# Performance work log

Measured on AMD Instinct MI355X. Metric: run time of the kernel, lower is better.

The kernel has to match this reference:

```python
import jax, jax.numpy as jnp
import numpy as np

N_NODES = 100000
N_EDGES = 600000
IN_DIM = 128
HID = 128


def setup_inputs() -> dict:
    key = jax.random.key(0)
    ks = jax.random.split(key, 9)
    x = jax.random.normal(ks[0], (N_NODES, IN_DIM), dtype=jnp.float32)
    edge_index = jax.random.randint(ks[1], (2, N_EDGES), 0, N_NODES, dtype=jnp.int64)
    s = 1.0 / np.sqrt(IN_DIM)
    # PyG SAGEConv: out = lin_l(mean_aggr(x_src)) + lin_r(x_root); lin_l carries the bias.
    W_l0 = jax.random.uniform(ks[2], (IN_DIM, HID), jnp.float32, -s, s)
    b_l0 = jnp.zeros((HID,), jnp.float32)
    W_r0 = jax.random.uniform(ks[3], (IN_DIM, HID), jnp.float32, -s, s)
    s2 = 1.0 / np.sqrt(HID)
    W_l1 = jax.random.uniform(ks[4], (HID, HID), jnp.float32, -s2, s2)
    b_l1 = jnp.zeros((HID,), jnp.float32)
    W_r1 = jax.random.uniform(ks[5], (HID, HID), jnp.float32, -s2, s2)
    return {"x": x, "edge_index": edge_index,
            "W_l0": W_l0, "b_l0": b_l0, "W_r0": W_r0,
            "W_l1": W_l1, "b_l1": b_l1, "W_r1": W_r1}


def _sage_mean_conv(h, src, dst, W_l, b_l, W_r):
    # gather source-node features per edge, scatter-mean into destinations
    msgs = h[src]                                              # [E, D]
    sums = jax.ops.segment_sum(msgs, dst, num_segments=N_NODES)  # [N, D]
    cnt = jax.ops.segment_sum(jnp.ones((src.shape[0],), h.dtype), dst,
                              num_segments=N_NODES)             # [N]
    mean = sums / jnp.maximum(cnt, 1.0)[:, None]
    return mean @ W_l + b_l + h @ W_r


def reference(x, edge_index, W_l0, b_l0, W_r0, W_l1, b_l1, W_r1):
    src, dst = edge_index[0], edge_index[1]
    h = _sage_mean_conv(x, src, dst, W_l0, b_l0, W_r0)
    h = jax.nn.relu(h)  # dropout is identity in eval mode
    h = _sage_mean_conv(h, src, dst, W_l1, b_l1, W_r1)
    h = jax.nn.relu(h)
    return h
```

## Files before the change

kernel.cpp:

```cpp
#include <hip/hip_runtime.h>

#define N_NODES 100000
#define N_EDGES 600000
#define DIM 128

typedef __attribute__((ext_vector_type(8))) short bf16x8;
typedef __attribute__((ext_vector_type(4))) float f32x4;

typedef __attribute__((address_space(1))) const unsigned int g_u32;
typedef __attribute__((address_space(3))) unsigned int l_u32;
__device__ __forceinline__ void stage16(const void* g, void* l) {
  __builtin_amdgcn_global_load_lds((g_u32*)g, (l_u32*)l, 16, 0, 0);
}

__device__ __forceinline__ unsigned short f32_to_bf16_rn(float f) {
  unsigned int u = __builtin_bit_cast(unsigned int, f);
  unsigned int r = (u + 0x7FFFu + ((u >> 16) & 1u)) >> 16;
  return (unsigned short)r;
}

__global__ __launch_bounds__(256) void prep_k(
    const float* __restrict__ Wl0, const float* __restrict__ Wr0,
    const float* __restrict__ Wl1, const float* __restrict__ Wr1,
    unsigned short* __restrict__ P0, unsigned short* __restrict__ P1,
    const float* __restrict__ x, unsigned short* __restrict__ xhi,
    int* __restrict__ deg) {
  const int gid = blockIdx.x * 256 + threadIdx.x;
  if (gid < N_NODES) deg[gid] = 0;
  if (gid < 65536) {
    const int layer = gid >> 15;
    const int idx = gid & 32767;
    const int j = idx & 7;
    const int l = (idx >> 3) & 63;
    const int nt = (idx >> 9) & 7;
    const int g = idx >> 12;
    const int k = ((g & 3) << 5) + ((l >> 4) << 3) + j;
    const int n = (nt << 4) + (l & 15);
    const float* W = layer ? ((g < 4) ? Wl1 : Wr1) : ((g < 4) ? Wl0 : Wr0);
    (layer ? P1 : P0)[idx] = f32_to_bf16_rn(W[k * 128 + n]);
  } else {
    const int i = gid - 65536;
    if (i < N_NODES * DIM / 4) {
      const float4 v = reinterpret_cast<const float4*>(x)[i];
      const float f[4] = {v.x, v.y, v.z, v.w};
      unsigned short h[4];
#pragma unroll
      for (int j = 0; j < 4; ++j) h[j] = f32_to_bf16_rn(f[j]);
      uint2 hp;
      hp.x = (unsigned)h[0] | ((unsigned)h[1] << 16);
      hp.y = (unsigned)h[2] | ((unsigned)h[3] << 16);
      reinterpret_cast<uint2*>(xhi)[i] = hp;
    }
  }
}

__global__ void hist_k(const int* __restrict__ dst, int* __restrict__ deg) {
  int e = blockIdx.x * blockDim.x + threadIdx.x;
  if (e < N_EDGES) atomicAdd(&deg[dst[e]], 1);
}

__global__ __launch_bounds__(1024) void scan1_k(const int* __restrict__ deg,
                                                int* __restrict__ incl,
                                                int* __restrict__ bsum) {
  __shared__ int wsum[16];
  const int t = threadIdx.x, lane = t & 63, w = t >> 6;
  const int gi = blockIdx.x * 1024 + t;
  int v = (gi < N_NODES) ? deg[gi] : 0;
  int s = v;
#pragma unroll
  for (int off = 1; off < 64; off <<= 1) {
    int u = __shfl_up(s, off);
    if (lane >= off) s += u;
  }
  if (lane == 63) wsum[w] = s;
  __syncthreads();
  if (t < 16) {
    int ws = wsum[t];
#pragma unroll
    for (int off = 1; off < 16; off <<= 1) {
      int u = __shfl_up(ws, off);
      if (t >= off) ws += u;
    }
    wsum[t] = ws;
  }
  __syncthreads();
  const int val = s + (w ? wsum[w - 1] : 0);
  if (gi < N_NODES) incl[gi] = val;
  if (t == 1023) bsum[blockIdx.x] = val;
}

__global__ void scan2_k(const int* __restrict__ bsum, int* __restrict__ boffs,
                        int nb) {
  __shared__ int w0;
  const int t = threadIdx.x;
  int v = (t < nb) ? bsum[t] : 0;
  int s = v;
#pragma unroll
  for (int off = 1; off < 64; off <<= 1) {
    int u = __shfl_up(s, off);
    if ((t & 63) >= off) s += u;
  }
  if (t == 63) w0 = s;
  __syncthreads();
  const int excl = s - v + ((t >> 6) ? w0 : 0);
  if (t < nb) boffs[t] = excl;
}

__global__ __launch_bounds__(1024) void scan3_k(const int* __restrict__ deg,
                                                const int* __restrict__ incl,
                                                const int* __restrict__ boffs,
                                                int* __restrict__ rowptr,
                                                int* __restrict__ head) {
  const int gi = blockIdx.x * 1024 + threadIdx.x;
  if (gi < N_NODES) {
    const int e = incl[gi] - deg[gi] + boffs[blockIdx.x];
    rowptr[gi] = e;
    head[gi] = e;
  }
  if (gi == 0) rowptr[N_NODES] = N_EDGES;
}

__global__ void fill_k(const int* __restrict__ src, const int* __restrict__ dst,
                       int* __restrict__ head, int* __restrict__ col) {
  int e = blockIdx.x * blockDim.x + threadIdx.x;
  if (e < N_EDGES) {
    int p = atomicAdd(&head[dst[e]], 1);
    col[p] = src[e];
  }
}

__global__ __launch_bounds__(256) void agg_k(
    const unsigned short* __restrict__ plane, const int* __restrict__ rowptr,
    const int* __restrict__ col, unsigned short* __restrict__ mhi) {
  const int t = threadIdx.x;
  const int node = blockIdx.x * 16 + (t >> 4);
  const int q = t & 15;
  const int beg = rowptr[node], end = rowptr[node + 1];
  const uint4* P = reinterpret_cast<const uint4*>(plane);
  float a[8] = {};

  auto accum = [&](uint4 v) {
    const unsigned int u[4] = {v.x, v.y, v.z, v.w};
#pragma unroll
    for (int w = 0; w < 4; ++w) {
      a[2 * w] += __builtin_bit_cast(float, u[w] << 16);
      a[2 * w + 1] += __builtin_bit_cast(float, u[w] & 0xFFFF0000u);
    }
  };

  for (int i = beg; i < end; i += 4) {
    const int i1 = min(i + 1, end - 1);
    const int i2 = min(i + 2, end - 1);
    const int i3 = min(i + 3, end - 1);
    const int c0 = col[i], c1 = col[i1], c2 = col[i2], c3 = col[i3];
    const uint4 v0 = P[(size_t)c0 * 16 + q];
    const uint4 v1 = P[(size_t)c1 * 16 + q];
    const uint4 v2 = P[(size_t)c2 * 16 + q];
    const uint4 v3 = P[(size_t)c3 * 16 + q];
    accum(v0);
    if (i + 1 < end) accum(v1);
    if (i + 2 < end) accum(v2);
    if (i + 3 < end) accum(v3);
  }

  const int d = end - beg;
  const float inv = 1.0f / (float)(d > 1 ? d : 1);
  unsigned int hw[4];
#pragma unroll
  for (int w = 0; w < 4; ++w) {
    const unsigned short h0 = f32_to_bf16_rn(a[2 * w] * inv);
    const unsigned short h1 = f32_to_bf16_rn(a[2 * w + 1] * inv);
    hw[w] = (unsigned)h0 | ((unsigned)h1 << 16);
  }
  uint4 ho = {hw[0], hw[1], hw[2], hw[3]};
  reinterpret_cast<uint4*>(mhi)[(size_t)node * 16 + q] = ho;
}

template <int OUTF32>
__global__ __launch_bounds__(256, 4) void gemm_k(
    const unsigned short* __restrict__ Mhi, const unsigned short* __restrict__ Hhi,
    const unsigned short* __restrict__ Bp, const float* __restrict__ bias,
    unsigned short* __restrict__ Ohi, float* __restrict__ Of) {
  __shared__ unsigned short Bl[2][4096];
  const int t = threadIdx.x;
  const int lane = t & 63;
  const int wid = t >> 6;
  const int rbase = blockIdx.x * 64 + wid * 16;
  const int lm = lane & 15, lk = lane >> 4;
  const size_t r0 = (size_t)min(rbase + lm, N_NODES - 1);

  f32x4 acc[8] = {};

  auto stageG = [&](int g, int nb) {
#pragma unroll
    for (int c = 0; c < 2; ++c) {
      const int e = (c * 256 + t) * 8;
      stage16(Bp + (size_t)g * 4096 + e, &Bl[nb][e]);
    }
  };
  auto loadA = [&](int g) {
    const unsigned short* P = (g < 4) ? Mhi : Hhi;
    const int ke = ((g & 3) << 5) + (lk << 3);
    return *reinterpret_cast<const bf16x8*>(P + r0 * DIM + ke);
  };

  stageG(0, 0);
  bf16x8 ca = loadA(0), na;
  __syncthreads();

#pragma unroll
  for (int g = 0; g < 8; ++g) {
    const int buf = g & 1;
    if (g < 7) {
      stageG(g + 1, buf ^ 1);
      na = loadA(g + 1);
    }
#pragma unroll
    for (int nt = 0; nt < 8; ++nt) {
      const bf16x8 b =
          *reinterpret_cast<const bf16x8*>(&Bl[buf][(nt * 64 + lane) * 8]);
      acc[nt] = __builtin_amdgcn_mfma_f32_16x16x32_bf16(ca, b, acc[nt], 0, 0, 0);
    }
    __syncthreads();
    ca = na;
  }

#pragma unroll
  for (int nt = 0; nt < 8; ++nt) {
    const int cidx = nt * 16 + lm;
    const float bv = bias[cidx];
#pragma unroll
    for (int i = 0; i < 4; ++i) {
      const int r = rbase + lk * 4 + i;
      if (r < N_NODES) {
        float v = acc[nt][i] + bv;
        v = fmaxf(v, 0.0f);
        if (OUTF32) {
          Of[(size_t)r * DIM + cidx] = v;
        } else {
          Ohi[(size_t)r * DIM + cidx] = f32_to_bf16_rn(v);
        }
      }
    }
  }
}

extern "C" void kernel_launch(void* const* d_in, const int* in_sizes, int n_in,
                              void* d_out, int out_size, void* d_ws,
                              size_t ws_size, hipStream_t stream) {
  const float* x = (const float*)d_in[0];
  const int* ei = (const int*)d_in[1];
  const float* Wl0 = (const float*)d_in[2];
  const float* bl0 = (const float*)d_in[3];
  const float* Wr0 = (const float*)d_in[4];
  const float* Wl1 = (const float*)d_in[5];
  const float* bl1 = (const float*)d_in[6];
  const float* Wr1 = (const float*)d_in[7];
  float* out = (float*)d_out;
  const int* src = ei;
  const int* dst = ei + N_EDGES;

  char* p = (char*)d_ws;
  auto alloc = [&](size_t bytes) {
    char* q = p;
    p += (bytes + 255) & ~(size_t)255;
    return q;
  };
  int* deg = (int*)alloc((size_t)N_NODES * 4);
  int* rowptr = (int*)alloc((size_t)(N_NODES + 1) * 4);
  int* head = (int*)alloc((size_t)N_NODES * 4);
  int* col = (int*)alloc((size_t)N_EDGES * 4);
  int* bsum = (int*)alloc(128 * 4);
  int* boffs = (int*)alloc(128 * 4);
  unsigned short* Bp0 = (unsigned short*)alloc(32768 * 2);
  unsigned short* Bp1 = (unsigned short*)alloc(32768 * 2);
  unsigned short* xhi = (unsigned short*)alloc((size_t)N_NODES * DIM * 2);
  unsigned short* mhi = (unsigned short*)alloc((size_t)N_NODES * DIM * 2);
  unsigned short* h1hi = (unsigned short*)alloc((size_t)N_NODES * DIM * 2);

  const int nScanB = (N_NODES + 1023) / 1024;

  prep_k<<<(65536 + N_NODES * DIM / 4 + 255) / 256, 256, 0, stream>>>(
      Wl0, Wr0, Wl1, Wr1, Bp0, Bp1, x, xhi, deg);
  hist_k<<<(N_EDGES + 255) / 256, 256, 0, stream>>>(dst, deg);
  scan1_k<<<nScanB, 1024, 0, stream>>>(deg, head, bsum);
  scan2_k<<<1, 128, 0, stream>>>(bsum, boffs, nScanB);
  scan3_k<<<nScanB, 1024, 0, stream>>>(deg, head, boffs, rowptr, head);
  fill_k<<<(N_EDGES + 255) / 256, 256, 0, stream>>>(src, dst, head, col);

  const int nBlocks = (N_NODES + 63) / 64;
  const int aggBlocks = N_NODES / 16;

  agg_k<<<aggBlocks, 256, 0, stream>>>(xhi, rowptr, col, mhi);
  gemm_k<0><<<nBlocks, 256, 0, stream>>>(mhi, xhi, Bp0, bl0, h1hi, nullptr);
  agg_k<<<aggBlocks, 256, 0, stream>>>(h1hi, rowptr, col, mhi);
  gemm_k<1><<<nBlocks, 256, 0, stream>>>(mhi, h1hi, Bp1, bl1, nullptr, out);
}
```

Before: 176.7 us.

## Fold block-offset scan into scan3 and double K-step prefetch in GEMM

Removes the separate single-block scan2 launch: each scan3 block now reduces the preceding block sums itself with a wave reduction, saving one kernel launch and its serialization. The GEMM moves from two to four LDS buffers and processes two K-groups per barrier, prefetching two groups of weights and activations ahead. This halves the barrier count and deepens prefetch, but doubles the LDS footprint and raises register pressure, which may reduce occupancy.

```diff
diff --git a/kernel.cpp b/kernel.cpp
--- a/kernel.cpp
+++ b/kernel.cpp
@@ -89,31 +89,26 @@
   if (t == 1023) bsum[blockIdx.x] = val;
 }
 
-__global__ void scan2_k(const int* __restrict__ bsum, int* __restrict__ boffs,
-                        int nb) {
-  __shared__ int w0;
-  const int t = threadIdx.x;
-  int v = (t < nb) ? bsum[t] : 0;
-  int s = v;
-#pragma unroll
-  for (int off = 1; off < 64; off <<= 1) {
-    int u = __shfl_up(s, off);
-    if ((t & 63) >= off) s += u;
-  }
-  if (t == 63) w0 = s;
-  __syncthreads();
-  const int excl = s - v + ((t >> 6) ? w0 : 0);
-  if (t < nb) boffs[t] = excl;
-}
-
 __global__ __launch_bounds__(1024) void scan3_k(const int* __restrict__ deg,
                                                 const int* __restrict__ incl,
-                                                const int* __restrict__ boffs,
+                                                const int* __restrict__ bsum,
                                                 int* __restrict__ rowptr,
                                                 int* __restrict__ head) {
-  const int gi = blockIdx.x * 1024 + threadIdx.x;
+  __shared__ int spart[2];
+  __shared__ int boff_s;
+  const int t = threadIdx.x;
+  if (t < 128) {
+    int v = (t < blockIdx.x) ? bsum[t] : 0;
+#pragma unroll
+    for (int off = 1; off < 64; off <<= 1) v += __shfl_xor(v, off);
+    if ((t & 63) == 0) spart[t >> 6] = v;
+  }
+  __syncthreads();
+  if (t == 0) boff_s = spart[0] + spart[1];
+  __syncthreads();
+  const int gi = blockIdx.x * 1024 + t;
   if (gi < N_NODES) {
-    const int e = incl[gi] - deg[gi] + boffs[blockIdx.x];
+    const int e = incl[gi] - deg[gi] + boff_s;
     rowptr[gi] = e;
     head[gi] = e;
   }
@@ -181,7 +176,7 @@
     const unsigned short* __restrict__ Mhi, const unsigned short* __restrict__ Hhi,
     const unsigned short* __restrict__ Bp, const float* __restrict__ bias,
     unsigned short* __restrict__ Ohi, float* __restrict__ Of) {
-  __shared__ unsigned short Bl[2][4096];
+  __shared__ unsigned short Bl[4][4096];
   const int t = threadIdx.x;
   const int lane = t & 63;
   const int wid = t >> 6;
@@ -205,24 +200,34 @@
   };
 
   stageG(0, 0);
-  bf16x8 ca = loadA(0), na;
-  __syncthreads();
-
-#pragma unroll
-  for (int g = 0; g < 8; ++g) {
-    const int buf = g & 1;
-    if (g < 7) {
-      stageG(g + 1, buf ^ 1);
-      na = loadA(g + 1);
+  stageG(1, 1);
+  bf16x8 ca0 = loadA(0), ca1 = loadA(1), na0, na1;
+  __syncthreads();
+
+#pragma unroll
+  for (int pg = 0; pg < 4; ++pg) {
+    const int b0 = (2 * pg) & 3, b1 = (2 * pg + 1) & 3;
+    if (pg < 3) {
+      stageG(2 * pg + 2, (b0 + 2) & 3);
+      stageG(2 * pg + 3, (b1 + 2) & 3);
+      na0 = loadA(2 * pg + 2);
+      na1 = loadA(2 * pg + 3);
     }
 #pragma unroll
     for (int nt = 0; nt < 8; ++nt) {
       const bf16x8 b =
-          *reinterpret_cast<const bf16x8*>(&Bl[buf][(nt * 64 + lane) * 8]);
-      acc[nt] = __builtin_amdgcn_mfma_f32_16x16x32_bf16(ca, b, acc[nt], 0, 0, 0);
+          *reinterpret_cast<const bf16x8*>(&Bl[b0][(nt * 64 + lane) * 8]);
+      acc[nt] = __builtin_amdgcn_mfma_f32_16x16x32_bf16(ca0, b, acc[nt], 0, 0, 0);
+    }
+#pragma unroll
+    for (int nt = 0; nt < 8; ++nt) {
+      const bf16x8 b =
+          *reinterpret_cast<const bf16x8*>(&Bl[b1][(nt * 64 + lane) * 8]);
+      acc[nt] = __builtin_amdgcn_mfma_f32_16x16x32_bf16(ca1, b, acc[nt], 0, 0, 0);
     }
     __syncthreads();
-    ca = na;
+    ca0 = na0;
+    ca1 = na1;
   }
 
 #pragma unroll
@@ -271,7 +276,6 @@
   int* head = (int*)alloc((size_t)N_NODES * 4);
   int* col = (int*)alloc((size_t)N_EDGES * 4);
   int* bsum = (int*)alloc(128 * 4);
-  int* boffs = (int*)alloc(128 * 4);
   unsigned short* Bp0 = (unsigned short*)alloc(32768 * 2);
   unsigned short* Bp1 = (unsigned short*)alloc(32768 * 2);
   unsigned short* xhi = (unsigned short*)alloc((size_t)N_NODES * DIM * 2);
@@ -284,8 +288,7 @@
       Wl0, Wr0, Wl1, Wr1, Bp0, Bp1, x, xhi, deg);
   hist_k<<<(N_EDGES + 255) / 256, 256, 0, stream>>>(dst, deg);
   scan1_k<<<nScanB, 1024, 0, stream>>>(deg, head, bsum);
-  scan2_k<<<1, 128, 0, stream>>>(bsum, boffs, nScanB);
-  scan3_k<<<nScanB, 1024, 0, stream>>>(deg, head, boffs, rowptr, head);
+  scan3_k<<<nScanB, 1024, 0, stream>>>(deg, head, bsum, rowptr, head);
   fill_k<<<(N_EDGES + 255) / 256, 256, 0, stream>>>(src, dst, head, col);
 
   const int nBlocks = (N_NODES + 63) / 64;
```

After: 182.0 us. 1.03x slower.
